# Kernel tuning notes

Hardware: AMD Instinct MI355X
Metric: run time of the kernel (lower is better)

## Reference

```python
import jax, jax.numpy as jnp
import numpy as np

N_FEATURE = 128
N_OUTPUT = 2  # number of GatedEquivariant layers
N_ATOMS = 100000
N_GRAPHS = 128


def setup_inputs() -> dict:
    key = jax.random.key(0)
    ks = jax.random.split(key, 16)
    F = N_FEATURE
    L = N_OUTPUT
    sc = 1.0 / np.sqrt(F)
    s = jax.random.normal(ks[0], (1, N_ATOMS, F), dtype=jnp.float32)
    v = jax.random.normal(ks[1], (1, N_ATOMS, 3, F), dtype=jnp.float32)
    r = jax.random.normal(ks[2], (1, N_ATOMS, 3), dtype=jnp.float32)
    # one-hot batch mask: each atom belongs to one of N_GRAPHS molecules
    seg = jnp.sort(jax.random.randint(ks[3], (N_ATOMS,), 0, N_GRAPHS))
    batch_mask = (seg[None, :] == jnp.arange(N_GRAPHS)[:, None]).astype(jnp.float32)[..., None]  # (B,N,1)
    # GatedEquivariant params, stacked over L layers; stored (in,out) so y = x @ W + b
    w1 = jax.random.normal(ks[4], (L, F, F), dtype=jnp.float32) * sc
    w2 = jax.random.normal(ks[5], (L, F, F), dtype=jnp.float32) * sc
    a1w = jax.random.normal(ks[6], (L, 2 * F, F), dtype=jnp.float32) * (1.0 / np.sqrt(2 * F))
    a1b = jnp.zeros((L, F), dtype=jnp.float32)
    a2w = jax.random.normal(ks[7], (L, F, 2 * F), dtype=jnp.float32) * sc
    a2b = jnp.zeros((L, 2 * F), dtype=jnp.float32)
    out_w = jax.random.normal(ks[8], (F, 1), dtype=jnp.float32) * sc
    out_b = jnp.zeros((1,), dtype=jnp.float32)
    return {"s": s, "v": v, "r": r, "batch_mask": batch_mask,
            "w1": w1, "w2": w2, "a1w": a1w, "a1b": a1b,
            "a2w": a2w, "a2b": a2b, "out_w": out_w, "out_b": out_b}


def _gated_equivariant(s, v, w1, w2, a1w, a1b, a2w, a2b):
    # v: (1,N,3,F); linear layers act on the feature (last) dim
    v1 = jnp.einsum('bncf,fg->bncg', v, w1)
    v2 = jnp.einsum('bncf,fg->bncg', v, w2)
    n2 = jnp.linalg.norm(v2, axis=-2)                 # (1,N,F) norm over spatial dim
    h = jnp.concatenate([s, n2], axis=-1)             # (1,N,2F)
    h = jax.nn.silu(h @ a1w + a1b)                    # (1,N,F)
    h = h @ a2w + a2b                                 # (1,N,2F)
    s_out, g = jnp.split(h, 2, axis=-1)
    v_out = g[..., None, :] * v1                      # gate broadcast over spatial dim
    return s_out, v_out


def reference(s, v, r, batch_mask, w1, w2, a1w, a1b, a2w, a2b, out_w, out_b):
    del r  # r only used when dy=True (not the case here)
    for i in range(w1.shape[0]):  # small fixed layer count
        s, v = _gated_equivariant(s, v, w1[i], w2[i], a1w[i], a1b[i], a2w[i], a2b[i])
    sc = s @ out_w + out_b                            # (1,N,1)
    # torch: (sc.repeat(B,1,1) * batch_mask).sum(-2) == masked segment-sum via broadcast
    y = jnp.sum(sc * batch_mask, axis=-2)             # (B,1)
    return y
```

## Files before the change

### kernel.cpp

```cpp
#include <hip/hip_runtime.h>
#include <hip/hip_bf16.h>

#define NF 128
#define NF2 256
#define NATOMS 100000
#define NGRAPH 128

#define MT 32
#define NBLK (NATOMS/MT)
#define NTHR 512

#define OW1 0
#define OW2 16384
#define OA1 32768
#define OA2 65536
#define LAYER_SZ 98304

typedef __attribute__((ext_vector_type(8))) short bf16x8;
typedef __attribute__((ext_vector_type(4))) short bf16x4;
typedef __attribute__((ext_vector_type(4))) float f32x4;

static __device__ __forceinline__ float bf2f(__hip_bfloat16 x) { return __bfloat162float(x); }
static __device__ __forceinline__ __hip_bfloat16 f2bf(float x) { return __float2bfloat16(x); }
static __device__ __forceinline__ unsigned short f2bfu(float x) {
  __hip_bfloat16 h = __float2bfloat16(x);
  return *(unsigned short*)&h;
}
static __device__ __forceinline__ bf16x8 pack8(float4 lo, float4 hi) {
  union { unsigned short s[8]; bf16x8 v; } u;
  u.s[0]=f2bfu(lo.x); u.s[1]=f2bfu(lo.y); u.s[2]=f2bfu(lo.z); u.s[3]=f2bfu(lo.w);
  u.s[4]=f2bfu(hi.x); u.s[5]=f2bfu(hi.y); u.s[6]=f2bfu(hi.z); u.s[7]=f2bfu(hi.w);
  return u.v;
}
static __device__ __forceinline__ bf16x4 pack4f(f32x4 a) {
  union { unsigned short s[4]; bf16x4 v; } u;
  u.s[0]=f2bfu(a[0]); u.s[1]=f2bfu(a[1]); u.s[2]=f2bfu(a[2]); u.s[3]=f2bfu(a[3]);
  return u.v;
}
static __device__ __forceinline__ float bfs2f(short s) {
  __hip_bfloat16 h; *(short*)&h = s; return __bfloat162float(h);
}

static __device__ __forceinline__ bf16x8 ldfrag(const __hip_bfloat16* buf, int gr, int row, int gi) {
  return *(const bf16x8*)&buf[(row*gr + (gi ^ (row & 7)))*8];
}
static __device__ __forceinline__ void stq(__hip_bfloat16* buf, int gr, int row, int colb, bf16x4 v) {
  int gi = colb >> 3, off = colb & 7;
  *(bf16x4*)&buf[(row*gr + (gi ^ (row & 7)))*8 + off] = v;
}
static __device__ __forceinline__ bf16x4 ldq(const __hip_bfloat16* buf, int gr, int row, int colb) {
  int gi = colb >> 3, off = colb & 7;
  return *(const bf16x4*)&buf[(row*gr + (gi ^ (row & 7)))*8 + off];
}
static __device__ __forceinline__ float ldb(const __hip_bfloat16* buf, int gr, int row, int col) {
  int gi = col >> 3, off = col & 7;
  return bf2f(buf[(row*gr + (gi ^ (row & 7)))*8 + off]);
}

__global__ __launch_bounds__(256)
void prep_weights(const float* __restrict__ w1, const float* __restrict__ w2,
                  const float* __restrict__ a1w, const float* __restrict__ a2w,
                  __hip_bfloat16* __restrict__ blob) {
  int gid = blockIdx.x * 256 + threadIdx.x;
  int layer = gid / 12288;
  int r = gid - layer * 12288;
  const float* W; int N, nks, g; __hip_bfloat16* dst;
  if (r < 2048)      { W = w1  + layer*NF*NF;  N = NF;  nks = 4; dst = blob + layer*LAYER_SZ + OW1; g = r; }
  else if (r < 4096) { W = w2  + layer*NF*NF;  N = NF;  nks = 4; dst = blob + layer*LAYER_SZ + OW2; g = r - 2048; }
  else if (r < 8192) { W = a1w + layer*NF2*NF; N = NF;  nks = 8; dst = blob + layer*LAYER_SZ + OA1; g = r - 4096; }
  else               { W = a2w + layer*NF*NF2; N = NF2; nks = 4; dst = blob + layer*LAYER_SZ + OA2; g = r - 8192; }
  int lane = g & 63;
  int ks = (g >> 6) % nks;
  int ct = g / (64 * nks);
  int k0 = ks * 32 + ((lane >> 4) << 3);
  int n  = ct * 16 + (lane & 15);
  __hip_bfloat16* o = dst + (size_t)((ct * nks + ks) * 64 + lane) * 8;
  #pragma unroll
  for (int j = 0; j < 8; ++j) o[j] = f2bf(W[(size_t)(k0 + j) * N + n]);
}

__global__ __launch_bounds__(NTHR, 4)
void fused_equiv(const float* __restrict__ s_g, const float* __restrict__ v_g,
                 const __hip_bfloat16* __restrict__ blob,
                 const float* __restrict__ a1b, const float* __restrict__ a2b,
                 const float* __restrict__ out_w, const float* __restrict__ out_b,
                 float* __restrict__ sc) {
  __shared__ __hip_bfloat16 vcur[3*MT*NF];
  __shared__ __hip_bfloat16 v1lds[3*MT*NF];
  __shared__ __hip_bfloat16 hbuf[MT*NF2];
  __shared__ __hip_bfloat16 h1[MT*NF];

  const int tid  = threadIdx.x;
  const int wave = tid >> 6;
  const int lane = tid & 63;
  const int l15  = lane & 15;
  const int quad = lane >> 4;
  const int a0   = blockIdx.x * MT;
  const int fb   = wave*16 + quad*4;

  {
    int row = tid >> 4, gi = tid & 15;
    const float* sp = s_g + (size_t)a0*NF + row*NF + gi*8;
    float4 lo = *(const float4*)sp;
    float4 hi = *(const float4*)(sp + 4);
    *(bf16x8*)&hbuf[(row*32 + (gi ^ (row & 7)))*8] = pack8(lo, hi);
    #pragma unroll
    for (int u = 0; u < 3; ++u) {
      int g = tid + u*512;
      int R = g >> 4, gi2 = g & 15;
      int at = R / 3, c = R - 3*at;
      const float* vp = v_g + (size_t)a0*3*NF + R*NF + gi2*8;
      float4 vlo = *(const float4*)vp;
      float4 vhi = *(const float4*)(vp + 4);
      *(bf16x8*)&vcur[((c*MT + at)*16 + (gi2 ^ (at & 7)))*8] = pack8(vlo, vhi);
    }
  }
  __syncthreads();

  const f32x4 b1a4  = *(const f32x4*)&a1b[fb];
  const f32x4 b1g4  = *(const f32x4*)&a1b[NF + fb];
  const f32x4 b2s4  = *(const f32x4*)&a2b[fb];
  const f32x4 b2g4  = *(const f32x4*)&a2b[NF + fb];
  const f32x4 b2s24 = *(const f32x4*)&a2b[2*NF + fb];

  {
    const __hip_bfloat16* lb = blob;
    bf16x8 wf[4];
    #pragma unroll
    for (int ks = 0; ks < 4; ++ks)
      wf[ks] = *(const bf16x8*)&lb[OW1 + ((size_t)(wave*4 + ks)*64 + lane)*8];
    #pragma unroll
    for (int rt = 0; rt < 2; ++rt) {
      int arow = rt*16 + l15;
      #pragma unroll
      for (int c = 0; c < 3; ++c) {
        f32x4 acc = {0.f,0.f,0.f,0.f};
        #pragma unroll
        for (int ks = 0; ks < 4; ++ks) {
          bf16x8 af = ldfrag(vcur + c*MT*NF, 16, arow, ks*4 + quad);
          acc = __builtin_amdgcn_mfma_f32_16x16x32_bf16(wf[ks], af, acc, 0, 0, 0);
        }
        stq(v1lds + c*MT*NF, 16, arow, fb, pack4f(acc));
      }
    }
  }
  {
    const __hip_bfloat16* lb = blob;
    bf16x8 wf[4];
    #pragma unroll
    for (int ks = 0; ks < 4; ++ks)
      wf[ks] = *(const bf16x8*)&lb[OW2 + ((size_t)(wave*4 + ks)*64 + lane)*8];
    #pragma unroll
    for (int rt = 0; rt < 2; ++rt) {
      int arow = rt*16 + l15;
      f32x4 nq = {0.f,0.f,0.f,0.f};
      #pragma unroll
      for (int c = 0; c < 3; ++c) {
        f32x4 acc = {0.f,0.f,0.f,0.f};
        #pragma unroll
        for (int ks = 0; ks < 4; ++ks) {
          bf16x8 af = ldfrag(vcur + c*MT*NF, 16, arow, ks*4 + quad);
          acc = __builtin_amdgcn_mfma_f32_16x16x32_bf16(wf[ks], af, acc, 0, 0, 0);
        }
        #pragma unroll
        for (int i = 0; i < 4; ++i) nq[i] += acc[i]*acc[i];
      }
      f32x4 nv;
      #pragma unroll
      for (int i = 0; i < 4; ++i) nv[i] = sqrtf(nq[i]);
      stq(hbuf, 32, arow, NF + fb, pack4f(nv));
    }
  }
  __syncthreads();

  {
    const __hip_bfloat16* lb = blob;
    bf16x8 a1f[8];
    #pragma unroll
    for (int ks = 0; ks < 8; ++ks)
      a1f[ks] = *(const bf16x8*)&lb[OA1 + ((size_t)(wave*8 + ks)*64 + lane)*8];
    #pragma unroll
    for (int rt = 0; rt < 2; ++rt) {
      int arow = rt*16 + l15;
      f32x4 acc = {0.f,0.f,0.f,0.f};
      #pragma unroll
      for (int ks = 0; ks < 8; ++ks) {
        bf16x8 af = ldfrag(hbuf, 32, arow, ks*4 + quad);
        acc = __builtin_amdgcn_mfma_f32_16x16x32_bf16(a1f[ks], af, acc, 0, 0, 0);
      }
      f32x4 h;
      #pragma unroll
      for (int i = 0; i < 4; ++i) {
        float x = acc[i] + b1a4[i];
        h[i] = x / (1.0f + __expf(-x));
      }
      stq(h1, 16, arow, fb, pack4f(h));
    }
  }
  __syncthreads();

  {
    const __hip_bfloat16* lb = blob;
    bf16x8 asf[4], agf[4];
    #pragma unroll
    for (int ks = 0; ks < 4; ++ks) {
      asf[ks] = *(const bf16x8*)&lb[OA2 + ((size_t)(wave*4 + ks)*64 + lane)*8];
      agf[ks] = *(const bf16x8*)&lb[OA2 + ((size_t)((wave+8)*4 + ks)*64 + lane)*8];
    }
    #pragma unroll
    for (int rt = 0; rt < 2; ++rt) {
      int arow = rt*16 + l15;
      f32x4 hs = {0.f,0.f,0.f,0.f}, hg = {0.f,0.f,0.f,0.f};
      #pragma unroll
      for (int ks = 0; ks < 4; ++ks) {
        bf16x8 af = ldfrag(h1, 16, arow, ks*4 + quad);
        hs = __builtin_amdgcn_mfma_f32_16x16x32_bf16(asf[ks], af, hs, 0, 0, 0);
        hg = __builtin_amdgcn_mfma_f32_16x16x32_bf16(agf[ks], af, hg, 0, 0, 0);
      }
      f32x4 sv, g;
      #pragma unroll
      for (int i = 0; i < 4; ++i) { sv[i] = hs[i] + b2s4[i]; g[i] = hg[i] + b2g4[i]; }
      stq(hbuf, 32, arow, fb, pack4f(sv));
      #pragma unroll
      for (int c = 0; c < 3; ++c) {
        bf16x4 vv = ldq(v1lds + c*MT*NF, 16, arow, fb);
        f32x4 gv;
        #pragma unroll
        for (int i = 0; i < 4; ++i) gv[i] = g[i] * bfs2f(vv[i]);
        stq(v1lds + c*MT*NF, 16, arow, fb, pack4f(gv));
      }
    }
  }
  __syncthreads();

  {
    const __hip_bfloat16* lb = blob + LAYER_SZ;
    bf16x8 wf[4];
    #pragma unroll
    for (int ks = 0; ks < 4; ++ks)
      wf[ks] = *(const bf16x8*)&lb[OW2 + ((size_t)(wave*4 + ks)*64 + lane)*8];
    #pragma unroll
    for (int rt = 0; rt < 2; ++rt) {
      int arow = rt*16 + l15;
      f32x4 nq = {0.f,0.f,0.f,0.f};
      #pragma unroll
      for (int c = 0; c < 3; ++c) {
        f32x4 acc = {0.f,0.f,0.f,0.f};
        #pragma unroll
        for (int ks = 0; ks < 4; ++ks) {
          bf16x8 af = ldfrag(v1lds + c*MT*NF, 16, arow, ks*4 + quad);
          acc = __builtin_amdgcn_mfma_f32_16x16x32_bf16(wf[ks], af, acc, 0, 0, 0);
        }
        #pragma unroll
        for (int i = 0; i < 4; ++i) nq[i] += acc[i]*acc[i];
      }
      f32x4 nv;
      #pragma unroll
      for (int i = 0; i < 4; ++i) nv[i] = sqrtf(nq[i]);
      stq(hbuf, 32, arow, NF + fb, pack4f(nv));
    }
  }
  __syncthreads();

  {
    const __hip_bfloat16* lb = blob + LAYER_SZ;
    bf16x8 a1f[8];
    #pragma unroll
    for (int ks = 0; ks < 8; ++ks)
      a1f[ks] = *(const bf16x8*)&lb[OA1 + ((size_t)(wave*8 + ks)*64 + lane)*8];
    #pragma unroll
    for (int rt = 0; rt < 2; ++rt) {
      int arow = rt*16 + l15;
      f32x4 acc = {0.f,0.f,0.f,0.f};
      #pragma unroll
      for (int ks = 0; ks < 8; ++ks) {
        bf16x8 af = ldfrag(hbuf, 32, arow, ks*4 + quad);
        acc = __builtin_amdgcn_mfma_f32_16x16x32_bf16(a1f[ks], af, acc, 0, 0, 0);
      }
      f32x4 h;
      #pragma unroll
      for (int i = 0; i < 4; ++i) {
        float x = acc[i] + b1g4[i];
        h[i] = x / (1.0f + __expf(-x));
      }
      stq(h1, 16, arow, fb, pack4f(h));
    }
  }
  __syncthreads();

  {
    const __hip_bfloat16* lb = blob + LAYER_SZ;
    bf16x8 asf[4];
    #pragma unroll
    for (int ks = 0; ks < 4; ++ks)
      asf[ks] = *(const bf16x8*)&lb[OA2 + ((size_t)(wave*4 + ks)*64 + lane)*8];
    #pragma unroll
    for (int rt = 0; rt < 2; ++rt) {
      int arow = rt*16 + l15;
      f32x4 hs = {0.f,0.f,0.f,0.f};
      #pragma unroll
      for (int ks = 0; ks < 4; ++ks) {
        bf16x8 af = ldfrag(h1, 16, arow, ks*4 + quad);
        hs = __builtin_amdgcn_mfma_f32_16x16x32_bf16(asf[ks], af, hs, 0, 0, 0);
      }
      f32x4 sv;
      #pragma unroll
      for (int i = 0; i < 4; ++i) sv[i] = hs[i] + b2s24[i];
      stq(hbuf, 32, arow, fb, pack4f(sv));
    }
  }
  __syncthreads();

  {
    int a   = tid >> 4;
    int sub = tid & 15;
    float p = 0.f;
    #pragma unroll
    for (int j = 0; j < 8; ++j) {
      int f = sub*8 + j;
      p += ldb(hbuf, 32, a, f) * out_w[f];
    }
    p += __shfl_down(p, 8, 16);
    p += __shfl_down(p, 4, 16);
    p += __shfl_down(p, 2, 16);
    p += __shfl_down(p, 1, 16);
    if (sub == 0) sc[a0 + a] = p + out_b[0];
  }
}

#define CHUNK 6256
__global__ __launch_bounds__(256)
void reduce_partial(const float* __restrict__ mask, const float* __restrict__ sc,
                    float* __restrict__ partial) {
  int b  = blockIdx.x >> 4;
  int ch = blockIdx.x & 15;
  int n0 = ch * CHUNK;
  int n1 = n0 + CHUNK; if (n1 > NATOMS) n1 = NATOMS;
  const float4* m4 = (const float4*)(mask + (size_t)b * NATOMS + n0);
  const float4* s4 = (const float4*)(sc + n0);
  int nq = (n1 - n0) >> 2;
  float acc = 0.f;
  for (int i = threadIdx.x; i < nq; i += 256) {
    float4 m = m4[i], s = s4[i];
    acc += m.x*s.x + m.y*s.y + m.z*s.z + m.w*s.w;
  }
  #pragma unroll
  for (int d = 32; d > 0; d >>= 1) acc += __shfl_down(acc, d, 64);
  __shared__ float red[4];
  if ((threadIdx.x & 63) == 0) red[threadIdx.x >> 6] = acc;
  __syncthreads();
  if (threadIdx.x == 0) partial[blockIdx.x] = red[0] + red[1] + red[2] + red[3];
}

__global__ void reduce_final(const float* __restrict__ partial, float* __restrict__ out) {
  int b = threadIdx.x;
  if (b < NGRAPH) {
    float s = 0.f;
    #pragma unroll
    for (int k = 0; k < 16; ++k) s += partial[b*16 + k];
    out[b] = s;
  }
}

extern "C" void kernel_launch(void* const* d_in, const int* in_sizes, int n_in,
                              void* d_out, int out_size, void* d_ws, size_t ws_size,
                              hipStream_t stream) {
  const float* s    = (const float*)d_in[0];
  const float* v    = (const float*)d_in[1];
  const float* mask = (const float*)d_in[3];
  const float* w1   = (const float*)d_in[4];
  const float* w2   = (const float*)d_in[5];
  const float* a1w  = (const float*)d_in[6];
  const float* a1b  = (const float*)d_in[7];
  const float* a2w  = (const float*)d_in[8];
  const float* a2b  = (const float*)d_in[9];
  const float* outw = (const float*)d_in[10];
  const float* outb = (const float*)d_in[11];

  char* ws = (char*)d_ws;
  __hip_bfloat16* blob = (__hip_bfloat16*)ws;
  float* sc      = (float*)(ws + (size_t)2*LAYER_SZ*2);
  float* partial = (float*)(ws + (size_t)2*LAYER_SZ*2 + NATOMS*4);

  prep_weights<<<96, 256, 0, stream>>>(w1, w2, a1w, a2w, blob);
  fused_equiv<<<NBLK, NTHR, 0, stream>>>(s, v, blob, a1b, a2b, outw, outb, sc);
  reduce_partial<<<NGRAPH*16, 256, 0, stream>>>(mask, sc, partial);
  reduce_final<<<1, 128, 0, stream>>>(partial, (float*)d_out);
}
```

Before: 359.1 us.

## Drop v1 LDS buffer by recomputing v1 after gate and raise occupancy

Reorders layer 1 so the norm of v@W2, the MLP and the gate are computed first, then v@W1 is computed and gated in registers and written back in place into vcur, eliminating the separate v1 LDS buffer. The LDS saving and narrower bias live ranges allow launch bounds of 6 blocks per SM instead of 4, aiming to hide latency through more occupancy. The final readout now loads a vectorized 8-element fragment instead of 8 scalar LDS reads. The in-place overwrite of vcur needs an extra barrier inside the channel loop, and tighter register limits may cause spills.

```diff
diff --git a/kernel.cpp b/kernel.cpp
--- a/kernel.cpp
+++ b/kernel.cpp
@@ -47,14 +47,6 @@
 static __device__ __forceinline__ void stq(__hip_bfloat16* buf, int gr, int row, int colb, bf16x4 v) {
   int gi = colb >> 3, off = colb & 7;
   *(bf16x4*)&buf[(row*gr + (gi ^ (row & 7)))*8 + off] = v;
-}
-static __device__ __forceinline__ bf16x4 ldq(const __hip_bfloat16* buf, int gr, int row, int colb) {
-  int gi = colb >> 3, off = colb & 7;
-  return *(const bf16x4*)&buf[(row*gr + (gi ^ (row & 7)))*8 + off];
-}
-static __device__ __forceinline__ float ldb(const __hip_bfloat16* buf, int gr, int row, int col) {
-  int gi = col >> 3, off = col & 7;
-  return bf2f(buf[(row*gr + (gi ^ (row & 7)))*8 + off]);
 }
 
 __global__ __launch_bounds__(256)
@@ -79,14 +71,13 @@
   for (int j = 0; j < 8; ++j) o[j] = f2bf(W[(size_t)(k0 + j) * N + n]);
 }
 
-__global__ __launch_bounds__(NTHR, 4)
+__global__ __launch_bounds__(NTHR, 6)
 void fused_equiv(const float* __restrict__ s_g, const float* __restrict__ v_g,
                  const __hip_bfloat16* __restrict__ blob,
                  const float* __restrict__ a1b, const float* __restrict__ a2b,
                  const float* __restrict__ out_w, const float* __restrict__ out_b,
                  float* __restrict__ sc) {
   __shared__ __hip_bfloat16 vcur[3*MT*NF];
-  __shared__ __hip_bfloat16 v1lds[3*MT*NF];
   __shared__ __hip_bfloat16 hbuf[MT*NF2];
   __shared__ __hip_bfloat16 h1[MT*NF];
 
@@ -117,21 +108,16 @@
   }
   __syncthreads();
 
-  const f32x4 b1a4  = *(const f32x4*)&a1b[fb];
-  const f32x4 b1g4  = *(const f32x4*)&a1b[NF + fb];
-  const f32x4 b2s4  = *(const f32x4*)&a2b[fb];
-  const f32x4 b2g4  = *(const f32x4*)&a2b[NF + fb];
-  const f32x4 b2s24 = *(const f32x4*)&a2b[2*NF + fb];
-
   {
     const __hip_bfloat16* lb = blob;
     bf16x8 wf[4];
     #pragma unroll
     for (int ks = 0; ks < 4; ++ks)
-      wf[ks] = *(const bf16x8*)&lb[OW1 + ((size_t)(wave*4 + ks)*64 + lane)*8];
-    #pragma unroll
-    for (int rt = 0; rt < 2; ++rt) {
-      int arow = rt*16 + l15;
+      wf[ks] = *(const bf16x8*)&lb[OW2 + ((size_t)(wave*4 + ks)*64 + lane)*8];
+    #pragma unroll
+    for (int rt = 0; rt < 2; ++rt) {
+      int arow = rt*16 + l15;
+      f32x4 nq = {0.f,0.f,0.f,0.f};
       #pragma unroll
       for (int c = 0; c < 3; ++c) {
         f32x4 acc = {0.f,0.f,0.f,0.f};
@@ -140,12 +126,117 @@
           bf16x8 af = ldfrag(vcur + c*MT*NF, 16, arow, ks*4 + quad);
           acc = __builtin_amdgcn_mfma_f32_16x16x32_bf16(wf[ks], af, acc, 0, 0, 0);
         }
-        stq(v1lds + c*MT*NF, 16, arow, fb, pack4f(acc));
-      }
-    }
-  }
+        #pragma unroll
+        for (int i = 0; i < 4; ++i) nq[i] += acc[i]*acc[i];
+      }
+      f32x4 nv;
+      #pragma unroll
+      for (int i = 0; i < 4; ++i) nv[i] = sqrtf(nq[i]);
+      stq(hbuf, 32, arow, NF + fb, pack4f(nv));
+    }
+  }
+  __syncthreads();
+
   {
     const __hip_bfloat16* lb = blob;
+    bf16x8 a1f[8];
+    #pragma unroll
+    for (int ks = 0; ks < 8; ++ks)
+      a1f[ks] = *(const bf16x8*)&lb[OA1 + ((size_t)(wave*8 + ks)*64 + lane)*8];
+    const f32x4 b1a4 = *(const f32x4*)&a1b[fb];
+    #pragma unroll
+    for (int rt = 0; rt < 2; ++rt) {
+      int arow = rt*16 + l15;
+      f32x4 acc = {0.f,0.f,0.f,0.f};
+      #pragma unroll
+      for (int ks = 0; ks < 8; ++ks) {
+        bf16x8 af = ldfrag(hbuf, 32, arow, ks*4 + quad);
+        acc = __builtin_amdgcn_mfma_f32_16x16x32_bf16(a1f[ks], af, acc, 0, 0, 0);
+      }
+      f32x4 h;
+      #pragma unroll
+      for (int i = 0; i < 4; ++i) {
+        float x = acc[i] + b1a4[i];
+        h[i] = x / (1.0f + __expf(-x));
+      }
+      stq(h1, 16, arow, fb, pack4f(h));
+    }
+  }
+  __syncthreads();
+
+  f32x4 g[2];
+  {
+    const __hip_bfloat16* lb = blob;
+    {
+      bf16x8 asf[4];
+      #pragma unroll
+      for (int ks = 0; ks < 4; ++ks)
+        asf[ks] = *(const bf16x8*)&lb[OA2 + ((size_t)(wave*4 + ks)*64 + lane)*8];
+      const f32x4 b2s4 = *(const f32x4*)&a2b[fb];
+      #pragma unroll
+      for (int rt = 0; rt < 2; ++rt) {
+        int arow = rt*16 + l15;
+        f32x4 hs = {0.f,0.f,0.f,0.f};
+        #pragma unroll
+        for (int ks = 0; ks < 4; ++ks) {
+          bf16x8 af = ldfrag(h1, 16, arow, ks*4 + quad);
+          hs = __builtin_amdgcn_mfma_f32_16x16x32_bf16(asf[ks], af, hs, 0, 0, 0);
+        }
+        f32x4 sv;
+        #pragma unroll
+        for (int i = 0; i < 4; ++i) sv[i] = hs[i] + b2s4[i];
+        stq(hbuf, 32, arow, fb, pack4f(sv));
+      }
+    }
+    {
+      bf16x8 agf[4];
+      #pragma unroll
+      for (int ks = 0; ks < 4; ++ks)
+        agf[ks] = *(const bf16x8*)&lb[OA2 + ((size_t)((wave+8)*4 + ks)*64 + lane)*8];
+      const f32x4 b2g4 = *(const f32x4*)&a2b[NF + fb];
+      #pragma unroll
+      for (int rt = 0; rt < 2; ++rt) {
+        int arow = rt*16 + l15;
+        f32x4 hg = {0.f,0.f,0.f,0.f};
+        #pragma unroll
+        for (int ks = 0; ks < 4; ++ks) {
+          bf16x8 af = ldfrag(h1, 16, arow, ks*4 + quad);
+          hg = __builtin_amdgcn_mfma_f32_16x16x32_bf16(agf[ks], af, hg, 0, 0, 0);
+        }
+        #pragma unroll
+        for (int i = 0; i < 4; ++i) g[rt][i] = hg[i] + b2g4[i];
+      }
+    }
+  }
+
+  {
+    const __hip_bfloat16* lb = blob;
+    bf16x8 wf[4];
+    #pragma unroll
+    for (int ks = 0; ks < 4; ++ks)
+      wf[ks] = *(const bf16x8*)&lb[OW1 + ((size_t)(wave*4 + ks)*64 + lane)*8];
+    #pragma unroll
+    for (int c = 0; c < 3; ++c) {
+      f32x4 acc0 = {0.f,0.f,0.f,0.f}, acc1 = {0.f,0.f,0.f,0.f};
+      #pragma unroll
+      for (int ks = 0; ks < 4; ++ks) {
+        bf16x8 af0 = ldfrag(vcur + c*MT*NF, 16, l15,      ks*4 + quad);
+        bf16x8 af1 = ldfrag(vcur + c*MT*NF, 16, 16 + l15, ks*4 + quad);
+        acc0 = __builtin_amdgcn_mfma_f32_16x16x32_bf16(wf[ks], af0, acc0, 0, 0, 0);
+        acc1 = __builtin_amdgcn_mfma_f32_16x16x32_bf16(wf[ks], af1, acc1, 0, 0, 0);
+      }
+      __syncthreads();
+      f32x4 gv0, gv1;
+      #pragma unroll
+      for (int i = 0; i < 4; ++i) { gv0[i] = g[0][i]*acc0[i]; gv1[i] = g[1][i]*acc1[i]; }
+      stq(vcur + c*MT*NF, 16, l15,      fb, pack4f(gv0));
+      stq(vcur + c*MT*NF, 16, 16 + l15, fb, pack4f(gv1));
+    }
+  }
+  __syncthreads();
+
+  {
+    const __hip_bfloat16* lb = blob + LAYER_SZ;
     bf16x8 wf[4];
     #pragma unroll
     for (int ks = 0; ks < 4; ++ks)
@@ -174,11 +265,12 @@
   __syncthreads();
 
   {
-    const __hip_bfloat16* lb = blob;
+    const __hip_bfloat16* lb = blob + LAYER_SZ;
     bf16x8 a1f[8];
     #pragma unroll
     for (int ks = 0; ks < 8; ++ks)
       a1f[ks] = *(const bf16x8*)&lb[OA1 + ((size_t)(wave*8 + ks)*64 + lane)*8];
+    const f32x4 b1g4 = *(const f32x4*)&a1b[NF + fb];
     #pragma unroll
     for (int rt = 0; rt < 2; ++rt) {
       int arow = rt*16 + l15;
@@ -191,7 +283,7 @@
       f32x4 h;
       #pragma unroll
       for (int i = 0; i < 4; ++i) {
-        float x = acc[i] + b1a4[i];
+        float x = acc[i] + b1g4[i];
         h[i] = x / (1.0f + __expf(-x));
       }
       stq(h1, 16, arow, fb, pack4f(h));
@@ -200,108 +292,20 @@
   __syncthreads();
 
   {
-    const __hip_bfloat16* lb = blob;
-    bf16x8 asf[4], agf[4];
-    #pragma unroll
-    for (int ks = 0; ks < 4; ++ks) {
+    const __hip_bfloat16* lb = blob + LAYER_SZ;
+    bf16x8 asf[4];
+    #pragma unroll
+    for (int ks = 0; ks < 4; ++ks)
       asf[ks] = *(const bf16x8*)&lb[OA2 + ((size_t)(wave*4 + ks)*64 + lane)*8];
-      agf[ks] = *(const bf16x8*)&lb[OA2 + ((size_t)((wave+8)*4 + ks)*64 + lane)*8];
-    }
-    #pragma unroll
-    for (int rt = 0; rt < 2; ++rt) {
-      int arow = rt*16 + l15;
-      f32x4 hs = {0.f,0.f,0.f,0.f}, hg = {0.f,0.f,0.f,0.f};
+    const f32x4 b2s24 = *(const f32x4*)&a2b[2*NF + fb];
+    #pragma unroll
+    for (int rt = 0; rt < 2; ++rt) {
+      int arow = rt*16 + l15;
+      f32x4 hs = {0.f,0.f,0.f,0.f};
       #pragma unroll
       for (int ks = 0; ks < 4; ++ks) {
         bf16x8 af = ldfrag(h1, 16, arow, ks*4 + quad);
         hs = __builtin_amdgcn_mfma_f32_16x16x32_bf16(asf[ks], af, hs, 0, 0, 0);
-        hg = __builtin_amdgcn_mfma_f32_16x16x32_bf16(agf[ks], af, hg, 0, 0, 0);
-      }
-      f32x4 sv, g;
-      #pragma unroll
-      for (int i = 0; i < 4; ++i) { sv[i] = hs[i] + b2s4[i]; g[i] = hg[i] + b2g4[i]; }
-      stq(hbuf, 32, arow, fb, pack4f(sv));
-      #pragma unroll
-      for (int c = 0; c < 3; ++c) {
-        bf16x4 vv = ldq(v1lds + c*MT*NF, 16, arow, fb);
-        f32x4 gv;
-        #pragma unroll
-        for (int i = 0; i < 4; ++i) gv[i] = g[i] * bfs2f(vv[i]);
-        stq(v1lds + c*MT*NF, 16, arow, fb, pack4f(gv));
-      }
-    }
-  }
-  __syncthreads();
-
-  {
-    const __hip_bfloat16* lb = blob + LAYER_SZ;
-    bf16x8 wf[4];
-    #pragma unroll
-    for (int ks = 0; ks < 4; ++ks)
-      wf[ks] = *(const bf16x8*)&lb[OW2 + ((size_t)(wave*4 + ks)*64 + lane)*8];
-    #pragma unroll
-    for (int rt = 0; rt < 2; ++rt) {
-      int arow = rt*16 + l15;
-      f32x4 nq = {0.f,0.f,0.f,0.f};
-      #pragma unroll
-      for (int c = 0; c < 3; ++c) {
-        f32x4 acc = {0.f,0.f,0.f,0.f};
-        #pragma unroll
-        for (int ks = 0; ks < 4; ++ks) {
-          bf16x8 af = ldfrag(v1lds + c*MT*NF, 16, arow, ks*4 + quad);
-          acc = __builtin_amdgcn_mfma_f32_16x16x32_bf16(wf[ks], af, acc, 0, 0, 0);
-        }
-        #pragma unroll
-        for (int i = 0; i < 4; ++i) nq[i] += acc[i]*acc[i];
-      }
-      f32x4 nv;
-      #pragma unroll
-      for (int i = 0; i < 4; ++i) nv[i] = sqrtf(nq[i]);
-      stq(hbuf, 32, arow, NF + fb, pack4f(nv));
-    }
-  }
-  __syncthreads();
-
-  {
-    const __hip_bfloat16* lb = blob + LAYER_SZ;
-    bf16x8 a1f[8];
-    #pragma unroll
-    for (int ks = 0; ks < 8; ++ks)
-      a1f[ks] = *(const bf16x8*)&lb[OA1 + ((size_t)(wave*8 + ks)*64 + lane)*8];
-    #pragma unroll
-    for (int rt = 0; rt < 2; ++rt) {
-      int arow = rt*16 + l15;
-      f32x4 acc = {0.f,0.f,0.f,0.f};
-      #pragma unroll
-      for (int ks = 0; ks < 8; ++ks) {
-        bf16x8 af = ldfrag(hbuf, 32, arow, ks*4 + quad);
-        acc = __builtin_amdgcn_mfma_f32_16x16x32_bf16(a1f[ks], af, acc, 0, 0, 0);
-      }
-      f32x4 h;
-      #pragma unroll
-      for (int i = 0; i < 4; ++i) {
-        float x = acc[i] + b1g4[i];
-        h[i] = x / (1.0f + __expf(-x));
-      }
-      stq(h1, 16, arow, fb, pack4f(h));
-    }
-  }
-  __syncthreads();
-
-  {
-    const __hip_bfloat16* lb = blob + LAYER_SZ;
-    bf16x8 asf[4];
-    #pragma unroll
-    for (int ks = 0; ks < 4; ++ks)
-      asf[ks] = *(const bf16x8*)&lb[OA2 + ((size_t)(wave*4 + ks)*64 + lane)*8];
-    #pragma unroll
-    for (int rt = 0; rt < 2; ++rt) {
-      int arow = rt*16 + l15;
-      f32x4 hs = {0.f,0.f,0.f,0.f};
-      #pragma unroll
-      for (int ks = 0; ks < 4; ++ks) {
-        bf16x8 af = ldfrag(h1, 16, arow, ks*4 + quad);
-        hs = __builtin_amdgcn_mfma_f32_16x16x32_bf16(asf[ks], af, hs, 0, 0, 0);
       }
       f32x4 sv;
       #pragma unroll
@@ -314,12 +318,11 @@
   {
     int a   = tid >> 4;
     int sub = tid & 15;
+    bf16x8 sv = ldfrag(hbuf, 32, a, sub);
+    const float* owp = out_w + sub*8;
     float p = 0.f;
     #pragma unroll
-    for (int j = 0; j < 8; ++j) {
-      int f = sub*8 + j;
-      p += ldb(hbuf, 32, a, f) * out_w[f];
-    }
+    for (int j = 0; j < 8; ++j) p += bfs2f(sv[j]) * owp[j];
     p += __shfl_down(p, 8, 16);
     p += __shfl_down(p, 4, 16);
     p += __shfl_down(p, 2, 16);
```

Measured after the change: 418.5 us. +16.5%, slower.
